# Kernel optimization log

Measured on AMD Instinct MI355X. Metric: run time of the kernel, lower is better.

The kernel has to match this reference:

```python
import jax, jax.numpy as jnp
import numpy as np

B, N_IN, NODE, L = 4, 128, 32, 256
N_HID, N_OUT = 64, 128
D_IN = N_HID          # d_inner = expand(1) * d_model
D_STATE = 2 * N_HID   # d_state = n_hid * 2
D_CONV = 2
DT_RANK = max(1, -(-N_HID // 16))  # ceil(d_model/16) = 4


def setup_inputs() -> dict:
    key = jax.random.key(0)
    ks = jax.random.split(key, 12)
    s = lambda k, shape, scale: (jax.random.normal(k, shape, jnp.float32) * scale)
    inputs = jax.random.normal(ks[0], (B, N_IN, NODE, L), jnp.float32)
    return {
        "inputs": inputs,
        "w_in": s(ks[1], (N_HID, N_IN), 1.0 / np.sqrt(N_IN)),
        "b_in": jnp.zeros((N_HID,), jnp.float32),
        "in_proj_w": s(ks[2], (2 * D_IN, N_HID), 1.0 / np.sqrt(N_HID)),
        "conv_w": s(ks[3], (D_IN, D_CONV), 0.5),
        "conv_b": jnp.zeros((D_IN,), jnp.float32),
        "x_proj_w": s(ks[4], (DT_RANK + 2 * D_STATE, D_IN), 1.0 / np.sqrt(D_IN)),
        "dt_proj_w": s(ks[5], (D_IN, DT_RANK), DT_RANK ** -0.5),
        "dt_proj_b": s(ks[6], (D_IN,), 0.1),
        "A_log": jnp.log(jnp.tile(jnp.arange(1, D_STATE + 1, dtype=jnp.float32)[None, :], (D_IN, 1))),
        "D": jnp.ones((D_IN,), jnp.float32),
        "out_proj_w": s(ks[7], (N_HID, D_IN), 1.0 / np.sqrt(D_IN)),
        "w_out": s(ks[8], (N_OUT, N_HID), 1.0 / np.sqrt(N_HID)),
        "b_out": jnp.zeros((N_OUT,), jnp.float32),
        "ln_w": jnp.ones((L, N_OUT), jnp.float32),
        "ln_b": jnp.zeros((L, N_OUT), jnp.float32),
    }


def _mamba(x, in_proj_w, conv_w, conv_b, x_proj_w, dt_proj_w, dt_proj_b, A_log, D, out_proj_w):
    # x: (Bseq, L, d_model)
    Bs, Ls, _ = x.shape
    d_state = A_log.shape[1]
    dt_rank = dt_proj_w.shape[1]
    d_conv = conv_w.shape[1]

    xz = x @ in_proj_w.T                     # (Bs, L, 2*d_inner)
    xm, z = jnp.split(xz, 2, axis=-1)

    # causal depthwise conv1d (padding = d_conv-1, truncated to L)
    xp = jnp.pad(xm, ((0, 0), (d_conv - 1, 0), (0, 0)))
    xc = sum(xp[:, k:k + Ls, :] * conv_w[:, k] for k in range(d_conv)) + conv_b
    xc = jax.nn.silu(xc)                     # (Bs, L, d_inner)

    dbc = xc @ x_proj_w.T                    # (Bs, L, dt_rank + 2*d_state)
    dt = dbc[..., :dt_rank]
    Bm = dbc[..., dt_rank:dt_rank + d_state]
    Cm = dbc[..., dt_rank + d_state:]
    delta = jax.nn.softplus(dt @ dt_proj_w.T + dt_proj_b)  # (Bs, L, d_inner)
    A = -jnp.exp(A_log)                      # (d_inner, d_state)

    def step(h, inp):
        dlt, Bt, Ct, xt = inp                # (Bs,d), (Bs,s), (Bs,s), (Bs,d)
        dA = jnp.exp(dlt[:, :, None] * A)    # (Bs, d, s)
        h = dA * h + (dlt * xt)[:, :, None] * Bt[:, None, :]
        y = jnp.einsum('bds,bs->bd', h, Ct)
        return h, y

    h0 = jnp.zeros((Bs, xm.shape[-1], d_state), x.dtype)
    xs = (delta.transpose(1, 0, 2), Bm.transpose(1, 0, 2),
          Cm.transpose(1, 0, 2), xc.transpose(1, 0, 2))
    _, ys = jax.lax.scan(step, h0, xs)       # ys: (L, Bs, d_inner)

    y = ys.transpose(1, 0, 2) + xc * D
    y = y * jax.nn.silu(z)
    return y @ out_proj_w.T                  # (Bs, L, d_model)


def reference(inputs, w_in, b_in, in_proj_w, conv_w, conv_b, x_proj_w,
              dt_proj_w, dt_proj_b, A_log, D, out_proj_w,
              w_out, b_out, ln_w, ln_b):
    b, n_in, node, seq = inputs.shape
    # permute(0,2,3,1).reshape(B*node, L, n_in)
    x = inputs.transpose(0, 2, 3, 1).reshape(b * node, seq, n_in)
    x = x @ w_in.T + b_in
    x = jax.nn.silu(_mamba(x, in_proj_w, conv_w, conv_b, x_proj_w,
                           dt_proj_w, dt_proj_b, A_log, D, out_proj_w))
    x = x @ w_out.T + b_out                  # (B*node, L, n_out)
    # LayerNorm over last two dims [feature_len, n_out]
    mu = x.mean(axis=(-2, -1), keepdims=True)
    var = ((x - mu) ** 2).mean(axis=(-2, -1), keepdims=True)
    x = (x - mu) / jnp.sqrt(var + 1e-5) * ln_w + ln_b
    return x.reshape(b, node, seq, -1).transpose(0, 3, 1, 2)
```

## Files before the change

kernel.cpp:

```cpp
#include <hip/hip_runtime.h>
#include <math.h>


__device__ __forceinline__ float silu_f(float v) { return v / (1.f + __expf(-v)); }
__device__ __forceinline__ float softplus_f(float v) { return v > 20.f ? v : log1pf(__expf(v)); }

__global__ __launch_bounds__(256) void k1_proj(
    const float* __restrict__ inp, const float* __restrict__ w_in,
    const float* __restrict__ b_in, const float* __restrict__ ipw,
    float* __restrict__ XM, float* __restrict__ Zb)
{
  __shared__ float sIN[128*64];
  __shared__ float sW[64*68];
  __shared__ float sXT[64*68];
  const int bid = blockIdx.x;
  const int r = bid >> 2, tb = bid & 3;
  const int b = r >> 5, node = r & 31;
  const int t0 = tb * 64;
  const int tid = threadIdx.x;
  const int tg = tid & 15, vg = tid >> 4;
  const int tl0 = tg * 4, v0 = vg * 4;

  for (int e = tid; e < 128*64; e += 256) {
    int i = e >> 6, t = e & 63;
    sIN[e] = inp[((b*128 + i)*32 + node)*256 + t0 + t];
  }

  float acc[4][4];
  #pragma unroll
  for (int ti = 0; ti < 4; ti++)
    #pragma unroll
    for (int j = 0; j < 4; j++) acc[ti][j] = b_in[v0 + j];

  for (int kc = 0; kc < 2; kc++) {
    __syncthreads();
    for (int e = tid; e < 64*16; e += 256) {
      int row = e >> 4, c4 = e & 15;
      *(float4*)&sW[row*68 + c4*4] = *(const float4*)&w_in[row*128 + kc*64 + c4*4];
    }
    __syncthreads();
    for (int k4 = 0; k4 < 16; k4++) {
      float4 wv[4];
      #pragma unroll
      for (int j = 0; j < 4; j++)
        wv[j] = *(const float4*)&sW[(v0 + j)*68 + k4*4];
      #pragma unroll
      for (int kk = 0; kk < 4; kk++) {
        float4 x4 = *(const float4*)&sIN[(kc*64 + k4*4 + kk)*64 + tl0];
        #pragma unroll
        for (int j = 0; j < 4; j++) {
          float w = kk==0 ? wv[j].x : kk==1 ? wv[j].y : kk==2 ? wv[j].z : wv[j].w;
          acc[0][j] = fmaf(x4.x, w, acc[0][j]);
          acc[1][j] = fmaf(x4.y, w, acc[1][j]);
          acc[2][j] = fmaf(x4.z, w, acc[2][j]);
          acc[3][j] = fmaf(x4.w, w, acc[3][j]);
        }
      }
    }
  }
  #pragma unroll
  for (int j = 0; j < 4; j++)
    *(float4*)&sXT[(v0 + j)*68 + tl0] =
        make_float4(acc[0][j], acc[1][j], acc[2][j], acc[3][j]);

  for (int pass = 0; pass < 2; pass++) {
    __syncthreads();
    for (int e = tid; e < 64*16; e += 256) {
      int row = e >> 4, c4 = e & 15;
      *(float4*)&sW[row*68 + c4*4] = *(const float4*)&ipw[(pass*64 + row)*64 + c4*4];
    }
    __syncthreads();

    float a2[4][4];
    #pragma unroll
    for (int ti = 0; ti < 4; ti++)
      #pragma unroll
      for (int j = 0; j < 4; j++) a2[ti][j] = 0.f;

    for (int k4 = 0; k4 < 16; k4++) {
      float4 wv[4];
      #pragma unroll
      for (int j = 0; j < 4; j++)
        wv[j] = *(const float4*)&sW[(v0 + j)*68 + k4*4];
      #pragma unroll
      for (int kk = 0; kk < 4; kk++) {
        float4 x4 = *(const float4*)&sXT[(k4*4 + kk)*68 + tl0];
        #pragma unroll
        for (int j = 0; j < 4; j++) {
          float w = kk==0 ? wv[j].x : kk==1 ? wv[j].y : kk==2 ? wv[j].z : wv[j].w;
          a2[0][j] = fmaf(x4.x, w, a2[0][j]);
          a2[1][j] = fmaf(x4.y, w, a2[1][j]);
          a2[2][j] = fmaf(x4.z, w, a2[2][j]);
          a2[3][j] = fmaf(x4.w, w, a2[3][j]);
        }
      }
    }

    float* dst = (pass == 0) ? XM : Zb;
    #pragma unroll
    for (int ti = 0; ti < 4; ti++)
      *(float4*)&dst[(r*256 + t0 + tl0 + ti)*64 + v0] =
          make_float4(a2[ti][0], a2[ti][1], a2[ti][2], a2[ti][3]);
  }
}

__global__ __launch_bounds__(256) void k2_conv_xproj(
    const float* __restrict__ XM, const float* __restrict__ convw,
    const float* __restrict__ convb, const float* __restrict__ xpw,
    const float* __restrict__ dtw, const float* __restrict__ dtb,
    float* __restrict__ XC, float* __restrict__ DELTA,
    float* __restrict__ BM, float* __restrict__ CM)
{
  __shared__ float sXM[65*64];
  __shared__ float sXC[64*68];
  __shared__ float sW[64*68];
  __shared__ float sDT[64*5];
  const int bid = blockIdx.x;
  const int r = bid >> 2, tb = bid & 3;
  const int t0 = tb * 64;
  const int tid = threadIdx.x;
  const int tg = tid & 15, vg = tid >> 4;
  const int tl0 = tg * 4, v0 = vg * 4;

  for (int e = tid; e < 65*64; e += 256) {
    int tt = e >> 6, d = e & 63;
    int tgl = t0 - 1 + tt;
    sXM[e] = (tgl < 0) ? 0.f : XM[(r*256 + tgl)*64 + d];
  }
  __syncthreads();

  for (int e = tid; e < 64*64; e += 256) {
    int t = e >> 6, d = e & 63;
    float c0 = convw[d*2], c1 = convw[d*2 + 1];
    float pre = fmaf(sXM[t*64 + d], c0, fmaf(sXM[(t+1)*64 + d], c1, convb[d]));
    float v = silu_f(pre);
    sXC[d*68 + t] = v;
    XC[(r*256 + t0 + t)*64 + d] = v;
  }

  for (int pass = 0; pass < 5; pass++) {
    __syncthreads();
    for (int e = tid; e < 64*16; e += 256) {
      int row = e >> 4, c4 = e & 15;
      int grow = pass*64 + row;
      float4 w = (grow < 260) ? *(const float4*)&xpw[grow*64 + c4*4]
                              : make_float4(0.f, 0.f, 0.f, 0.f);
      *(float4*)&sW[row*68 + c4*4] = w;
    }
    __syncthreads();

    float acc[4][4];
    #pragma unroll
    for (int ti = 0; ti < 4; ti++)
      #pragma unroll
      for (int jj = 0; jj < 4; jj++) acc[ti][jj] = 0.f;

    for (int k4 = 0; k4 < 16; k4++) {
      float4 wv[4];
      #pragma unroll
      for (int jj = 0; jj < 4; jj++)
        wv[jj] = *(const float4*)&sW[(v0 + jj)*68 + k4*4];
      #pragma unroll
      for (int kk = 0; kk < 4; kk++) {
        float4 x4 = *(const float4*)&sXC[(k4*4 + kk)*68 + tl0];
        #pragma unroll
        for (int jj = 0; jj < 4; jj++) {
          float w = kk==0 ? wv[jj].x : kk==1 ? wv[jj].y : kk==2 ? wv[jj].z : wv[jj].w;
          acc[0][jj] = fmaf(x4.x, w, acc[0][jj]);
          acc[1][jj] = fmaf(x4.y, w, acc[1][jj]);
          acc[2][jj] = fmaf(x4.z, w, acc[2][jj]);
          acc[3][jj] = fmaf(x4.w, w, acc[3][jj]);
        }
      }
    }

    const int j0g = pass*64 + v0;
    if (j0g < 4) {
      #pragma unroll
      for (int ti = 0; ti < 4; ti++)
        #pragma unroll
        for (int jj = 0; jj < 4; jj++)
          sDT[(tl0 + ti)*5 + jj] = acc[ti][jj];
    } else if (j0g < 132) {
      #pragma unroll
      for (int ti = 0; ti < 4; ti++)
        *(float4*)&BM[(r*256 + t0 + tl0 + ti)*128 + (j0g - 4)] =
            make_float4(acc[ti][0], acc[ti][1], acc[ti][2], acc[ti][3]);
    } else if (j0g < 260) {
      #pragma unroll
      for (int ti = 0; ti < 4; ti++)
        *(float4*)&CM[(r*256 + t0 + tl0 + ti)*128 + (j0g - 132)] =
            make_float4(acc[ti][0], acc[ti][1], acc[ti][2], acc[ti][3]);
    }
  }
  __syncthreads();

  for (int e = tid; e < 64*64; e += 256) {
    int t = e >> 6, d = e & 63;
    float4 w4 = *(const float4*)&dtw[d*4];
    float x = dtb[d];
    x = fmaf(sDT[t*5 + 0], w4.x, x);
    x = fmaf(sDT[t*5 + 1], w4.y, x);
    x = fmaf(sDT[t*5 + 2], w4.z, x);
    x = fmaf(sDT[t*5 + 3], w4.w, x);
    DELTA[(r*256 + t0 + t)*64 + d] = softplus_f(x);
  }
}

__global__ __launch_bounds__(256) void k3_scan(
    const float* __restrict__ DELTA, const float* __restrict__ XC,
    const float* __restrict__ BM, const float* __restrict__ CM,
    const float* __restrict__ alog, float* __restrict__ YP)
{
  __shared__ float sT[2*2560];
  const int bid = blockIdx.x;
  const int r = bid & 127;
  const int rest = bid >> 7;
  const int sc = rest & 1;
  const int dc = rest >> 1;
  const int tid = threadIdx.x;
  const int dg = tid >> 4;
  const int sg = tid & 15;
  const int sl0 = sg * 4;
  const int d = dc*16 + dg;
  const int sbase = sc*64 + sl0;
  const float LOG2E = 1.44269504f;

  float a2[4], h[4];
  #pragma unroll
  for (int j = 0; j < 4; j++) {
    a2[j] = -expf(alog[d*128 + sbase + j]) * LOG2E;
    h[j] = 0.f;
  }

  const float* baseB = BM + r*256*128 + sc*64;
  const float* baseC = CM + r*256*128 + sc*64;
  const float* baseD = DELTA + r*256*64 + dc*16;
  const float* baseX = XC + r*256*64 + dc*16;

  const int rowB = tid >> 6, colB = tid & 63;
  const int rowD = tid >> 4, colD = tid & 15;
  float pB[4], pC[4], pD, pX;

  #define K3_LOADT(T_) do { \
    int t0_ = (T_)*16; \
    pB[0] = baseB[(t0_ + rowB     )*128 + colB]; \
    pB[1] = baseB[(t0_ + rowB +  4)*128 + colB]; \
    pB[2] = baseB[(t0_ + rowB +  8)*128 + colB]; \
    pB[3] = baseB[(t0_ + rowB + 12)*128 + colB]; \
    pC[0] = baseC[(t0_ + rowB     )*128 + colB]; \
    pC[1] = baseC[(t0_ + rowB +  4)*128 + colB]; \
    pC[2] = baseC[(t0_ + rowB +  8)*128 + colB]; \
    pC[3] = baseC[(t0_ + rowB + 12)*128 + colB]; \
    pD = baseD[(t0_ + rowD)*64 + colD]; \
    pX = baseX[(t0_ + rowD)*64 + colD]; \
  } while (0)

  #define K3_STORET(BUF_) do { \
    float* S_ = &sT[(BUF_)*2560]; \
    S_[(rowB     )*64 + colB] = pB[0]; \
    S_[(rowB +  4)*64 + colB] = pB[1]; \
    S_[(rowB +  8)*64 + colB] = pB[2]; \
    S_[(rowB + 12)*64 + colB] = pB[3]; \
    S_[1024 + (rowB     )*64 + colB] = pC[0]; \
    S_[1024 + (rowB +  4)*64 + colB] = pC[1]; \
    S_[1024 + (rowB +  8)*64 + colB] = pC[2]; \
    S_[1024 + (rowB + 12)*64 + colB] = pC[3]; \
    S_[2048 + rowD*16 + colD] = pD; \
    S_[2304 + rowD*16 + colD] = pX; \
  } while (0)

  K3_LOADT(0);
  K3_STORET(0);
  K3_LOADT(1);
  __syncthreads();

  for (int k = 0; k < 16; k++) {
    if (k < 15) K3_STORET((k + 1) & 1);
    if (k < 14) K3_LOADT(k + 2);

    const float* S = &sT[(k & 1)*2560];
    #pragma unroll
    for (int tt = 0; tt < 16; tt++) {
      float dl = S[2048 + tt*16 + dg];
      float xv = S[2304 + tt*16 + dg];
      float u  = dl * xv;
      float4 Bv = *(const float4*)&S[tt*64 + sl0];
      float4 Cv = *(const float4*)&S[1024 + tt*64 + sl0];
      float y;
      {
        float dA0 = exp2f(dl * a2[0]);
        h[0] = fmaf(dA0, h[0], u * Bv.x);
        y = h[0] * Cv.x;
        float dA1 = exp2f(dl * a2[1]);
        h[1] = fmaf(dA1, h[1], u * Bv.y);
        y = fmaf(h[1], Cv.y, y);
        float dA2 = exp2f(dl * a2[2]);
        h[2] = fmaf(dA2, h[2], u * Bv.z);
        y = fmaf(h[2], Cv.z, y);
        float dA3 = exp2f(dl * a2[3]);
        h[3] = fmaf(dA3, h[3], u * Bv.w);
        y = fmaf(h[3], Cv.w, y);
      }
      y += __shfl_xor(y, 1);
      y += __shfl_xor(y, 2);
      y += __shfl_xor(y, 4);
      y += __shfl_xor(y, 8);
      if (sg == 0)
        YP[((sc*128 + r)*256 + k*16 + tt)*64 + d] = y;
    }

    __syncthreads();
  }
  #undef K3_LOADT
  #undef K3_STORET
}

__global__ __launch_bounds__(256) void k4_post(
    const float* __restrict__ YP, const float* __restrict__ XC,
    const float* __restrict__ Zb, const float* __restrict__ Dp,
    const float* __restrict__ opw, const float* __restrict__ wout,
    const float* __restrict__ bout, float* __restrict__ out,
    float* __restrict__ PSTAT)
{
  __shared__ float sY[64*68];
  __shared__ float sU[64*68];
  __shared__ float sW[64*68];
  __shared__ float sRs[256], sRq[256];
  const int bid = blockIdx.x;
  const int r = bid >> 2, tb = bid & 3;
  const int b = r >> 5, node = r & 31;
  const int t0 = tb * 64;
  const int tid = threadIdx.x;
  const int tg = tid & 15, vg = tid >> 4;
  const int tl0 = tg * 4, v0 = vg * 4;

  for (int e = tid; e < 64*64; e += 256) {
    int t = e >> 6, d = e & 63;
    int idx = (r*256 + t0 + t)*64 + d;
    float y = YP[idx] + YP[2097152 + idx];
    float y2 = fmaf(XC[idx], Dp[d], y);
    sY[d*68 + t] = y2 * silu_f(Zb[idx]);
  }

  __syncthreads();
  for (int e = tid; e < 64*16; e += 256) {
    int row = e >> 4, c4 = e & 15;
    *(float4*)&sW[row*68 + c4*4] = *(const float4*)&opw[row*64 + c4*4];
  }
  __syncthreads();

  {
    float acc[4][4];
    #pragma unroll
    for (int ti = 0; ti < 4; ti++)
      #pragma unroll
      for (int j = 0; j < 4; j++) acc[ti][j] = 0.f;
    for (int k4 = 0; k4 < 16; k4++) {
      float4 wv[4];
      #pragma unroll
      for (int j = 0; j < 4; j++)
        wv[j] = *(const float4*)&sW[(v0 + j)*68 + k4*4];
      #pragma unroll
      for (int kk = 0; kk < 4; kk++) {
        float4 x4 = *(const float4*)&sY[(k4*4 + kk)*68 + tl0];
        #pragma unroll
        for (int j = 0; j < 4; j++) {
          float w = kk==0 ? wv[j].x : kk==1 ? wv[j].y : kk==2 ? wv[j].z : wv[j].w;
          acc[0][j] = fmaf(x4.x, w, acc[0][j]);
          acc[1][j] = fmaf(x4.y, w, acc[1][j]);
          acc[2][j] = fmaf(x4.z, w, acc[2][j]);
          acc[3][j] = fmaf(x4.w, w, acc[3][j]);
        }
      }
    }
    #pragma unroll
    for (int j = 0; j < 4; j++)
      *(float4*)&sU[(v0 + j)*68 + tl0] =
          make_float4(silu_f(acc[0][j]), silu_f(acc[1][j]),
                      silu_f(acc[2][j]), silu_f(acc[3][j]));
  }

  float s = 0.f, q = 0.f;
  for (int pass = 0; pass < 2; pass++) {
    __syncthreads();
    for (int e = tid; e < 64*16; e += 256) {
      int row = e >> 4, c4 = e & 15;
      *(float4*)&sW[row*68 + c4*4] = *(const float4*)&wout[(pass*64 + row)*64 + c4*4];
    }
    __syncthreads();

    float a2[4][4];
    #pragma unroll
    for (int ti = 0; ti < 4; ti++)
      #pragma unroll
      for (int j = 0; j < 4; j++) a2[ti][j] = bout[pass*64 + v0 + j];

    for (int k4 = 0; k4 < 16; k4++) {
      float4 wv[4];
      #pragma unroll
      for (int j = 0; j < 4; j++)
        wv[j] = *(const float4*)&sW[(v0 + j)*68 + k4*4];
      #pragma unroll
      for (int kk = 0; kk < 4; kk++) {
        float4 x4 = *(const float4*)&sU[(k4*4 + kk)*68 + tl0];
        #pragma unroll
        for (int j = 0; j < 4; j++) {
          float w = kk==0 ? wv[j].x : kk==1 ? wv[j].y : kk==2 ? wv[j].z : wv[j].w;
          a2[0][j] = fmaf(x4.x, w, a2[0][j]);
          a2[1][j] = fmaf(x4.y, w, a2[1][j]);
          a2[2][j] = fmaf(x4.z, w, a2[2][j]);
          a2[3][j] = fmaf(x4.w, w, a2[3][j]);
        }
      }
    }

    #pragma unroll
    for (int ti = 0; ti < 4; ti++)
      #pragma unroll
      for (int j = 0; j < 4; j++) {
        float v = a2[ti][j];
        s += v;
        q = fmaf(v, v, q);
      }
    #pragma unroll
    for (int j = 0; j < 4; j++) {
      int o = pass*64 + v0 + j;
      *(float4*)&out[((b*128 + o)*32 + node)*256 + t0 + tl0] =
          make_float4(a2[0][j], a2[1][j], a2[2][j], a2[3][j]);
    }
  }

  sRs[tid] = s; sRq[tid] = q;
  __syncthreads();
  for (int st = 128; st > 0; st >>= 1) {
    if (tid < st) { sRs[tid] += sRs[tid + st]; sRq[tid] += sRq[tid + st]; }
    __syncthreads();
  }
  if (tid == 0) { PSTAT[bid*2] = sRs[0]; PSTAT[bid*2 + 1] = sRq[0]; }
}

__global__ __launch_bounds__(256) void k5_ln(
    const float* __restrict__ PSTAT, const float* __restrict__ lnw,
    const float* __restrict__ lnb, float* __restrict__ out)
{
  __shared__ float sLW[32*129], sLB[32*129];
  const int bid = blockIdx.x;
  const int r = bid >> 3, tb = bid & 7;
  const int b = r >> 5, node = r & 31;
  const int t0 = tb * 32;
  const int tid = threadIdx.x;

  float s = 0.f, q = 0.f;
  #pragma unroll
  for (int p = 0; p < 4; p++) {
    s += PSTAT[(r*4 + p)*2];
    q += PSTAT[(r*4 + p)*2 + 1];
  }
  const float mu = s * (1.f / 32768.f);
  const float var = q * (1.f / 32768.f) - mu * mu;
  const float rstd = rsqrtf(var + 1e-5f);

  for (int e = tid; e < 32*128; e += 256) {
    int t = e >> 7, o = e & 127;
    sLW[t*129 + o] = lnw[(t0 + t)*128 + o];
    sLB[t*129 + o] = lnb[(t0 + t)*128 + o];
  }
  __syncthreads();

  for (int n = 0; n < 16; n++) {
    int t = tid & 31;
    int o = (tid >> 5) + n*8;
    int idx = ((b*128 + o)*32 + node)*256 + t0 + t;
    float v = out[idx];
    out[idx] = fmaf((v - mu) * rstd, sLW[t*129 + o], sLB[t*129 + o]);
  }
}

extern "C" void kernel_launch(void* const* d_in, const int* in_sizes, int n_in,
                              void* d_out, int out_size, void* d_ws, size_t ws_size,
                              hipStream_t stream)
{
  (void)in_sizes; (void)n_in; (void)out_size; (void)ws_size;
  const float* inp   = (const float*)d_in[0];
  const float* w_in  = (const float*)d_in[1];
  const float* b_in  = (const float*)d_in[2];
  const float* ipw   = (const float*)d_in[3];
  const float* convw = (const float*)d_in[4];
  const float* convb = (const float*)d_in[5];
  const float* xpw   = (const float*)d_in[6];
  const float* dtw   = (const float*)d_in[7];
  const float* dtb   = (const float*)d_in[8];
  const float* alog  = (const float*)d_in[9];
  const float* Dp    = (const float*)d_in[10];
  const float* opw   = (const float*)d_in[11];
  const float* wout  = (const float*)d_in[12];
  const float* bout  = (const float*)d_in[13];
  const float* lnw   = (const float*)d_in[14];
  const float* lnb   = (const float*)d_in[15];

  float* ws = (float*)d_ws;
  float* XM    = ws + 0;
  float* Zb    = ws + 2097152;
  float* XC    = ws + 4194304;
  float* DELTA = ws + 6291456;
  float* BM    = ws + 8388608;
  float* CM    = ws + 12582912;
  float* YP    = ws + 16777216;
  float* PSTAT = ws + 20971520;
  float* out   = (float*)d_out;

  k1_proj<<<dim3(512), dim3(256), 0, stream>>>(inp, w_in, b_in, ipw, XM, Zb);
  k2_conv_xproj<<<dim3(512), dim3(256), 0, stream>>>(XM, convw, convb, xpw, dtw, dtb,
                                                     XC, DELTA, BM, CM);
  k3_scan<<<dim3(1024), dim3(256), 0, stream>>>(DELTA, XC, BM, CM, alog, YP);
  k4_post<<<dim3(512), dim3(256), 0, stream>>>(YP, XC, Zb, Dp, opw, wout, bout, out, PSTAT);
  k5_ln<<<dim3(1024), dim3(256), 0, stream>>>(PSTAT, lnw, lnb, out);
}
```

Baseline: 198.4 us.

## Drop LDS staging in scan kernel and reduce with DPP row rotates

The selective-scan kernel no longer double-buffers B, C, delta and x tiles through shared memory with per-tile barriers. Each thread now reads its float4 of B/C and its delta/x scalars straight from global memory (through the caches) inside an unroll-by-4 time loop. The 16-lane reduction of y switches from __shfl_xor to DPP row_ror adds, which avoids LDS permute traffic. The cost is that global-load latency now sits directly on the serial recurrence, and B/C rows are re-read by many threads instead of being shared through LDS.

```diff
diff --git a/kernel.cpp b/kernel.cpp
--- a/kernel.cpp
+++ b/kernel.cpp
@@ -212,7 +212,6 @@
     const float* __restrict__ BM, const float* __restrict__ CM,
     const float* __restrict__ alog, float* __restrict__ YP)
 {
-  __shared__ float sT[2*2560];
   const int bid = blockIdx.x;
   const int r = bid & 127;
   const int rest = bid >> 7;
@@ -223,97 +222,61 @@
   const int sg = tid & 15;
   const int sl0 = sg * 4;
   const int d = dc*16 + dg;
-  const int sbase = sc*64 + sl0;
   const float LOG2E = 1.44269504f;
 
   float a2[4], h[4];
   #pragma unroll
   for (int j = 0; j < 4; j++) {
-    a2[j] = -expf(alog[d*128 + sbase + j]) * LOG2E;
+    a2[j] = -expf(alog[d*128 + sc*64 + sl0 + j]) * LOG2E;
     h[j] = 0.f;
   }
 
-  const float* baseB = BM + r*256*128 + sc*64;
-  const float* baseC = CM + r*256*128 + sc*64;
-  const float* baseD = DELTA + r*256*64 + dc*16;
-  const float* baseX = XC + r*256*64 + dc*16;
-
-  const int rowB = tid >> 6, colB = tid & 63;
-  const int rowD = tid >> 4, colD = tid & 15;
-  float pB[4], pC[4], pD, pX;
-
-  #define K3_LOADT(T_) do { \
-    int t0_ = (T_)*16; \
-    pB[0] = baseB[(t0_ + rowB     )*128 + colB]; \
-    pB[1] = baseB[(t0_ + rowB +  4)*128 + colB]; \
-    pB[2] = baseB[(t0_ + rowB +  8)*128 + colB]; \
-    pB[3] = baseB[(t0_ + rowB + 12)*128 + colB]; \
-    pC[0] = baseC[(t0_ + rowB     )*128 + colB]; \
-    pC[1] = baseC[(t0_ + rowB +  4)*128 + colB]; \
-    pC[2] = baseC[(t0_ + rowB +  8)*128 + colB]; \
-    pC[3] = baseC[(t0_ + rowB + 12)*128 + colB]; \
-    pD = baseD[(t0_ + rowD)*64 + colD]; \
-    pX = baseX[(t0_ + rowD)*64 + colD]; \
-  } while (0)
-
-  #define K3_STORET(BUF_) do { \
-    float* S_ = &sT[(BUF_)*2560]; \
-    S_[(rowB     )*64 + colB] = pB[0]; \
-    S_[(rowB +  4)*64 + colB] = pB[1]; \
-    S_[(rowB +  8)*64 + colB] = pB[2]; \
-    S_[(rowB + 12)*64 + colB] = pB[3]; \
-    S_[1024 + (rowB     )*64 + colB] = pC[0]; \
-    S_[1024 + (rowB +  4)*64 + colB] = pC[1]; \
-    S_[1024 + (rowB +  8)*64 + colB] = pC[2]; \
-    S_[1024 + (rowB + 12)*64 + colB] = pC[3]; \
-    S_[2048 + rowD*16 + colD] = pD; \
-    S_[2304 + rowD*16 + colD] = pX; \
-  } while (0)
-
-  K3_LOADT(0);
-  K3_STORET(0);
-  K3_LOADT(1);
-  __syncthreads();
-
-  for (int k = 0; k < 16; k++) {
-    if (k < 15) K3_STORET((k + 1) & 1);
-    if (k < 14) K3_LOADT(k + 2);
-
-    const float* S = &sT[(k & 1)*2560];
-    #pragma unroll
-    for (int tt = 0; tt < 16; tt++) {
-      float dl = S[2048 + tt*16 + dg];
-      float xv = S[2304 + tt*16 + dg];
-      float u  = dl * xv;
-      float4 Bv = *(const float4*)&S[tt*64 + sl0];
-      float4 Cv = *(const float4*)&S[1024 + tt*64 + sl0];
-      float y;
-      {
-        float dA0 = exp2f(dl * a2[0]);
-        h[0] = fmaf(dA0, h[0], u * Bv.x);
-        y = h[0] * Cv.x;
-        float dA1 = exp2f(dl * a2[1]);
-        h[1] = fmaf(dA1, h[1], u * Bv.y);
-        y = fmaf(h[1], Cv.y, y);
-        float dA2 = exp2f(dl * a2[2]);
-        h[2] = fmaf(dA2, h[2], u * Bv.z);
-        y = fmaf(h[2], Cv.z, y);
-        float dA3 = exp2f(dl * a2[3]);
-        h[3] = fmaf(dA3, h[3], u * Bv.w);
-        y = fmaf(h[3], Cv.w, y);
-      }
-      y += __shfl_xor(y, 1);
-      y += __shfl_xor(y, 2);
-      y += __shfl_xor(y, 4);
-      y += __shfl_xor(y, 8);
-      if (sg == 0)
-        YP[((sc*128 + r)*256 + k*16 + tt)*64 + d] = y;
-    }
-
-    __syncthreads();
-  }
-  #undef K3_LOADT
-  #undef K3_STORET
+  const float* pB = BM    + r*256*128 + sc*64 + sl0;
+  const float* pC = CM    + r*256*128 + sc*64 + sl0;
+  const float* pD = DELTA + r*256*64  + d;
+  const float* pX = XC    + r*256*64  + d;
+  float*       pY = YP + ((size_t)(sc*128 + r))*256*64 + d;
+
+  #pragma unroll 4
+  for (int t = 0; t < 256; t++) {
+    float4 Bv = *(const float4*)(pB + t*128);
+    float4 Cv = *(const float4*)(pC + t*128);
+    float dl = pD[t*64];
+    float xv = pX[t*64];
+    float u = dl * xv;
+    float y;
+    {
+      float dA0 = exp2f(dl * a2[0]);
+      h[0] = fmaf(dA0, h[0], u * Bv.x);
+      y = h[0] * Cv.x;
+      float dA1 = exp2f(dl * a2[1]);
+      h[1] = fmaf(dA1, h[1], u * Bv.y);
+      y = fmaf(h[1], Cv.y, y);
+      float dA2 = exp2f(dl * a2[2]);
+      h[2] = fmaf(dA2, h[2], u * Bv.z);
+      y = fmaf(h[2], Cv.z, y);
+      float dA3 = exp2f(dl * a2[3]);
+      h[3] = fmaf(dA3, h[3], u * Bv.w);
+      y = fmaf(h[3], Cv.w, y);
+    }
+    {
+      int yi;
+      yi = __builtin_amdgcn_update_dpp(__float_as_int(y), __float_as_int(y),
+                                       0x121, 0xf, 0xf, false);
+      y += __int_as_float(yi);
+      yi = __builtin_amdgcn_update_dpp(__float_as_int(y), __float_as_int(y),
+                                       0x122, 0xf, 0xf, false);
+      y += __int_as_float(yi);
+      yi = __builtin_amdgcn_update_dpp(__float_as_int(y), __float_as_int(y),
+                                       0x124, 0xf, 0xf, false);
+      y += __int_as_float(yi);
+      yi = __builtin_amdgcn_update_dpp(__float_as_int(y), __float_as_int(y),
+                                       0x128, 0xf, 0xf, false);
+      y += __int_as_float(yi);
+    }
+    if (sg == 0)
+      pY[t*64] = y;
+  }
 }
 
 __global__ __launch_bounds__(256) void k4_post(
```

After: 212.4 us. 1.07x slower.
